# Performance work log

Measured on AMD Instinct MI355X. Metric: run time of the kernel, lower is better.

Reference implementation:

```python
import jax, jax.numpy as jnp
import numpy as np

N, E, F_IN, H, G, C = 100000, 1600000, 128, 128, 2048, 1
BN_EPS = 1e-5


def setup_inputs() -> dict:
    key = jax.random.key(0)
    ks = jax.random.split(key, 12)
    x = jax.random.normal(ks[0], (N, F_IN), dtype=jnp.float32)
    edge_index = jax.random.randint(ks[1], (2, E), 0, N, dtype=jnp.int64)
    batch = jnp.sort(jax.random.randint(ks[2], (N,), 0, G, dtype=jnp.int64))

    def xavier(k, fan_in, fan_out):
        lim = float(np.sqrt(6.0 / (fan_in + fan_out)))
        return jax.random.uniform(k, (fan_in, fan_out), jnp.float32, -lim, lim)

    return {
        "x": x, "edge_index": edge_index, "batch": batch,
        "W1": xavier(ks[3], F_IN, H), "b1": jnp.zeros((H,), jnp.float32),
        "g1": jnp.ones((H,), jnp.float32), "bt1": jnp.zeros((H,), jnp.float32),
        "W2": xavier(ks[4], H, H), "b2": jnp.zeros((H,), jnp.float32),
        "g2": jnp.ones((H,), jnp.float32), "bt2": jnp.zeros((H,), jnp.float32),
        "W3": xavier(ks[5], H, H), "b3": jnp.zeros((H,), jnp.float32),
        "g3": jnp.ones((H,), jnp.float32), "bt3": jnp.zeros((H,), jnp.float32),
        "fcw1": xavier(ks[6], H, H // 2), "fcb1": jnp.zeros((H // 2,), jnp.float32),
        "fcw2": xavier(ks[7], H // 2, C), "fcb2": jnp.zeros((C,), jnp.float32),
    }


def _gcn(x, W, b, src, dst, dis):
    # GCNConv: linear, then symmetric-normalized scatter-add with self-loops.
    xw = x @ W + b                                   # [N, H]
    norm = (dis[src] * dis[dst])[:, None]            # [E, 1]
    agg = jax.ops.segment_sum(xw[src] * norm, dst, num_segments=N)
    return agg + xw * (dis * dis)[:, None]           # self-loop term d^-1


def _bn(x, g, bt):
    mu = jnp.mean(x, axis=0)
    var = jnp.mean((x - mu) ** 2, axis=0)            # biased, training-mode BN
    return (x - mu) * jax.lax.rsqrt(var + BN_EPS) * g + bt


def reference(x, edge_index, batch, W1, b1, g1, bt1, W2, b2, g2, bt2,
              W3, b3, g3, bt3, fcw1, fcb1, fcw2, fcb2):
    src, dst = edge_index[0], edge_index[1]
    # degree with self-loops (counted on destination, as in PyG gcn_norm)
    deg = jax.ops.segment_sum(jnp.ones((E,), jnp.float32), dst, num_segments=N) + 1.0
    dis = jax.lax.rsqrt(deg)                         # deg^-1/2, deg >= 1

    h = jax.nn.relu(_bn(_gcn(x, W1, b1, src, dst, dis), g1, bt1))
    h = jax.nn.relu(_bn(_gcn(h, W2, b2, src, dst, dis), g2, bt2))
    h = jax.nn.relu(_bn(_gcn(h, W3, b3, src, dst, dis), g3, bt3))

    # global mean pool per graph
    sums = jax.ops.segment_sum(h, batch, num_segments=G)
    cnts = jax.ops.segment_sum(jnp.ones((N,), jnp.float32), batch, num_segments=G)
    pooled = sums / jnp.maximum(cnts, 1.0)[:, None]  # [G, H]

    out = jax.nn.relu(pooled @ fcw1 + fcb1)          # dropout is identity at eval
    return out @ fcw2 + fcb2                         # [G, C]
```

## Files before the change

kernel.cpp:

```cpp
#include <hip/hip_runtime.h>
#include <math.h>

#define Nn 100000
#define Ee 1600000
#define Gg 2048
#define HH 128
#define BN_EPS 1e-5f

#define NBK 196
#define NBLK_E 500
#define CHUNK4 800
#define NSTATB 256

typedef unsigned int uint32;
typedef unsigned char uchar_t;
typedef unsigned short ushort_t;
typedef __attribute__((ext_vector_type(8))) short short8_t;
typedef __attribute__((ext_vector_type(8))) unsigned short ushort8_t;
typedef __attribute__((ext_vector_type(4))) float f32x4_t;

__device__ __forceinline__ ushort_t f2bf(float f) {
    union { float f; uint32 u; } c; c.f = f;
    uint32 r = (c.u + 0x7FFFu + ((c.u >> 16) & 1u)) >> 16;
    return (ushort_t)r;
}
__device__ __forceinline__ float bflo(uint32 v) {
    union { uint32 u; float f; } c; c.u = v << 16; return c.f;
}
__device__ __forceinline__ float bfhi(uint32 v) {
    union { uint32 u; float f; } c; c.u = v & 0xFFFF0000u; return c.f;
}
__device__ __forceinline__ int q8(float f, float inv) {
    float t = f * inv;
    t = fmaxf(fminf(t, 127.f), -127.f);
    return (int)rintf(t);
}

__global__ __launch_bounds__(256) void k_count(const int* __restrict__ dst,
                                               int* __restrict__ blkhist) {
    __shared__ unsigned h[NBK];
    int tid = threadIdx.x;
    for (int i = tid; i < NBK; i += 256) h[i] = 0;
    __syncthreads();
    const int4* d4 = (const int4*)dst + blockIdx.x * CHUNK4;
    for (int i = tid; i < CHUNK4; i += 256) {
        int4 v = d4[i];
        atomicAdd(&h[v.x >> 9], 1u);
        atomicAdd(&h[v.y >> 9], 1u);
        atomicAdd(&h[v.z >> 9], 1u);
        atomicAdd(&h[v.w >> 9], 1u);
    }
    __syncthreads();
    for (int i = tid; i < NBK; i += 256)
        blkhist[blockIdx.x * NBK + i] = (int)h[i];
}

__global__ __launch_bounds__(512) void k_bscan1(const int* __restrict__ blkhist,
                                                int* __restrict__ blkoff_rel,
                                                int* __restrict__ total) {
    __shared__ int tmp[512];
    int bucket = blockIdx.x;
    int t = threadIdx.x;
    int v = (t < NBLK_E) ? blkhist[t * NBK + bucket] : 0;
    tmp[t] = v;
    __syncthreads();
    for (int off = 1; off < 512; off <<= 1) {
        int u = (t >= off) ? tmp[t - off] : 0;
        __syncthreads();
        tmp[t] += u;
        __syncthreads();
    }
    if (t < NBLK_E) blkoff_rel[t * NBK + bucket] = tmp[t] - v;
    if (t == 511) total[bucket] = tmp[t];
}

__global__ void k_bscan2(const int* __restrict__ total,
                         int* __restrict__ bucket_base) {
    __shared__ int tmp[256];
    int t = threadIdx.x;
    int v = (t < NBK) ? total[t] : 0;
    tmp[t] = v;
    __syncthreads();
    for (int off = 1; off < 256; off <<= 1) {
        int u = (t >= off) ? tmp[t - off] : 0;
        __syncthreads();
        tmp[t] += u;
        __syncthreads();
    }
    if (t < NBK) bucket_base[t] = tmp[t] - v;
}

__global__ __launch_bounds__(256) void k_fill1(const int* __restrict__ src,
                                               const int* __restrict__ dst,
                                               const int* __restrict__ bucket_base,
                                               const int* __restrict__ blkoff_rel,
                                               uint32* __restrict__ pairs) {
    __shared__ int loff[NBK];
    __shared__ unsigned lh[NBK];
    int tid = threadIdx.x;
    for (int i = tid; i < NBK; i += 256) {
        loff[i] = bucket_base[i] + blkoff_rel[blockIdx.x * NBK + i];
        lh[i] = 0;
    }
    __syncthreads();
    const int4* s4 = (const int4*)src + blockIdx.x * CHUNK4;
    const int4* d4 = (const int4*)dst + blockIdx.x * CHUNK4;
    for (int i = tid; i < CHUNK4; i += 256) {
        int4 s = s4[i];
        int4 d = d4[i];
        int b0 = d.x >> 9; int r0 = (int)atomicAdd(&lh[b0], 1u);
        pairs[loff[b0] + r0] = ((uint32)(d.x & 511) << 17) | (uint32)s.x;
        int b1 = d.y >> 9; int r1 = (int)atomicAdd(&lh[b1], 1u);
        pairs[loff[b1] + r1] = ((uint32)(d.y & 511) << 17) | (uint32)s.y;
        int b2 = d.z >> 9; int r2 = (int)atomicAdd(&lh[b2], 1u);
        pairs[loff[b2] + r2] = ((uint32)(d.z & 511) << 17) | (uint32)s.z;
        int b3 = d.w >> 9; int r3 = (int)atomicAdd(&lh[b3], 1u);
        pairs[loff[b3] + r3] = ((uint32)(d.w & 511) << 17) | (uint32)s.w;
    }
}

__global__ __launch_bounds__(1024) void k_fill2(const int* __restrict__ bucket_base,
                                                const int* __restrict__ total,
                                                const uint32* __restrict__ pairs,
                                                int* __restrict__ csr_src,
                                                int* __restrict__ rowptr,
                                                float* __restrict__ dis) {
    __shared__ unsigned lcnt[512];
    __shared__ int tmp[512];
    __shared__ int lcur[512];
    int b = blockIdx.x;
    int node0 = b * 512;
    int tid = threadIdx.x;
    for (int i = tid; i < 512; i += 1024) lcnt[i] = 0;
    __syncthreads();
    int beg = bucket_base[b];
    int endp = beg + total[b];
    for (int j = beg + tid; j < endp; j += 1024)
        atomicAdd(&lcnt[pairs[j] >> 17], 1u);
    __syncthreads();
    if (tid < 512) tmp[tid] = (int)lcnt[tid];
    __syncthreads();
    for (int off = 1; off < 512; off <<= 1) {
        int u = (tid < 512 && tid >= off) ? tmp[tid - off] : 0;
        __syncthreads();
        if (tid < 512) tmp[tid] += u;
        __syncthreads();
    }
    if (tid < 512) {
        int excl = tmp[tid] - (int)lcnt[tid];
        int n = node0 + tid;
        if (n <= Nn) rowptr[n] = beg + excl;
        if (n < Nn) dis[n] = rsqrtf((float)lcnt[tid] + 1.0f);
        lcur[tid] = beg + excl;
    }
    __syncthreads();
    for (int j = beg + tid; j < endp; j += 1024) {
        uint32 p = pairs[j];
        int dl = (int)(p >> 17);
        int s = (int)(p & 0x1FFFFu);
        int pos = atomicAdd(&lcur[dl], 1);
        csr_src[pos] = s;
    }
}

__global__ __launch_bounds__(256) void k_wprep(const float* __restrict__ W1,
                                               const float* __restrict__ W2,
                                               const float* __restrict__ W3,
                                               ushort_t* __restrict__ Wb) {
    int l = blockIdx.x >> 6, part = blockIdx.x & 63;
    const float* W = (l == 0) ? W1 : (l == 1) ? W2 : W3;
    int i = part * 256 + threadIdx.x;
    int k = i >> 7, col = i & 127;
    Wb[l * 16384 + col * 128 + k] = f2bf(W[k * 128 + col]);
}

__global__ __launch_bounds__(256) void k_gemm(const float* __restrict__ Xf,
                                              const uint32* __restrict__ Xb,
                                              const ushort_t* __restrict__ Wb,
                                              const float* __restrict__ Bv,
                                              const float* __restrict__ bnp,
                                              const float* __restrict__ dis,
                                              uchar_t* __restrict__ XW8,
                                              float* __restrict__ sc_src) {
    __shared__ ushort_t Wlds[128 * 136];
    __shared__ ushort_t Xlds[64 * 136];
    __shared__ float smax[64];
    const int tid = threadIdx.x;
    const int rowbase = blockIdx.x * 64;

#pragma unroll
    for (int it = 0; it < 8; ++it) {
        int chunk = tid + it * 256;
        int col = chunk >> 4, kg = chunk & 15;
        *(ushort8_t*)&Wlds[col * 136 + kg * 8] =
            *(const ushort8_t*)&Wb[col * 128 + kg * 8];
    }
    {
        int row = tid >> 2, q = tid & 3;
        int g = rowbase + row;
        if (bnp == nullptr) {
            const float4* Xr = (const float4*)(Xf + (size_t)g * 128);
#pragma unroll
            for (int it = 0; it < 8; ++it) {
                int c4 = q + it * 4;
                float4 v;
                if (g < Nn) v = Xr[c4];
                else { v.x = v.y = v.z = v.w = 0.f; }
                ushort4 o;
                o.x = f2bf(v.x); o.y = f2bf(v.y); o.z = f2bf(v.z); o.w = f2bf(v.w);
                *(ushort4*)&Xlds[row * 136 + c4 * 4] = o;
            }
        } else {
            const uint4* Hr = (const uint4*)(Xb + (size_t)g * 64);
#pragma unroll
            for (int it = 0; it < 4; ++it) {
                int i4 = q + it * 4;
                int c0 = i4 * 8;
                ushort8_t o;
                if (g < Nn) {
                    uint4 u = Hr[i4];
                    float4 sca = *(const float4*)&bnp[c0];
                    float4 scb = *(const float4*)&bnp[c0 + 4];
                    float4 sha = *(const float4*)&bnp[128 + c0];
                    float4 shb = *(const float4*)&bnp[128 + c0 + 4];
                    o[0] = f2bf(fmaxf(fmaf(bflo(u.x), sca.x, sha.x), 0.f));
                    o[1] = f2bf(fmaxf(fmaf(bfhi(u.x), sca.y, sha.y), 0.f));
                    o[2] = f2bf(fmaxf(fmaf(bflo(u.y), sca.z, sha.z), 0.f));
                    o[3] = f2bf(fmaxf(fmaf(bfhi(u.y), sca.w, sha.w), 0.f));
                    o[4] = f2bf(fmaxf(fmaf(bflo(u.z), scb.x, shb.x), 0.f));
                    o[5] = f2bf(fmaxf(fmaf(bfhi(u.z), scb.y, shb.y), 0.f));
                    o[6] = f2bf(fmaxf(fmaf(bflo(u.w), scb.z, shb.z), 0.f));
                    o[7] = f2bf(fmaxf(fmaf(bfhi(u.w), scb.w, shb.w), 0.f));
                } else {
                    for (int j = 0; j < 8; ++j) o[j] = 0;
                }
                *(ushort8_t*)&Xlds[row * 136 + c0] = o;
            }
        }
    }
    __syncthreads();

    const int wid = tid >> 6, lane = tid & 63;
    const int arow = wid * 16 + (lane & 15);
    const int koff = (lane >> 4) * 8;
    const int bcol = lane & 15;

    f32x4_t acc[8];
#pragma unroll
    for (int nt = 0; nt < 8; ++nt) acc[nt] = (f32x4_t){0.f, 0.f, 0.f, 0.f};

#pragma unroll
    for (int kt = 0; kt < 4; ++kt) {
        short8_t a = *(const short8_t*)&Xlds[arow * 136 + kt * 32 + koff];
#pragma unroll
        for (int nt = 0; nt < 8; ++nt) {
            short8_t b = *(const short8_t*)&Wlds[(nt * 16 + bcol) * 136 + kt * 32 + koff];
            acc[nt] = __builtin_amdgcn_mfma_f32_16x16x32_bf16(a, b, acc[nt], 0, 0, 0);
        }
    }

    int er = wid * 16 + (lane >> 4) * 4;
    int r0 = rowbase + er;
    float dv[4];
#pragma unroll
    for (int i = 0; i < 4; ++i) dv[i] = (r0 + i < Nn) ? dis[r0 + i] : 0.f;
    __syncthreads();
    float bs[8];
#pragma unroll
    for (int nt = 0; nt < 8; ++nt) bs[nt] = Bv[nt * 16 + bcol];
#pragma unroll
    for (int i = 0; i < 4; ++i) {
        float m = 0.f;
#pragma unroll
        for (int nt = 0; nt < 8; ++nt) {
            float v = (acc[nt][i] + bs[nt]) * dv[i];
            m = fmaxf(m, fabsf(v));
            Xlds[(er + i) * 136 + nt * 16 + bcol] = f2bf(v);
        }
        m = fmaxf(m, __shfl_xor(m, 1));
        m = fmaxf(m, __shfl_xor(m, 2));
        m = fmaxf(m, __shfl_xor(m, 4));
        m = fmaxf(m, __shfl_xor(m, 8));
        if (bcol == 0) smax[er + i] = m;
    }
    __syncthreads();
#pragma unroll
    for (int it = 0; it < 4; ++it) {
        int chunk = tid + it * 256;
        int row = chunk >> 4, cg = chunk & 15;
        int g = rowbase + row;
        if (g < Nn) {
            float mx = smax[row];
            float inv = (mx > 0.f) ? (127.0f / mx) : 0.f;
            uint4 u = *(const uint4*)&Xlds[row * 136 + cg * 8];
            int b0 = q8(bflo(u.x), inv), b1 = q8(bfhi(u.x), inv);
            int b2 = q8(bflo(u.y), inv), b3 = q8(bfhi(u.y), inv);
            int b4 = q8(bflo(u.z), inv), b5 = q8(bfhi(u.z), inv);
            int b6 = q8(bflo(u.w), inv), b7 = q8(bfhi(u.w), inv);
            uint2 o;
            o.x = (uint32)(b0 & 255) | ((uint32)(b1 & 255) << 8) |
                  ((uint32)(b2 & 255) << 16) | ((uint32)(b3 & 255) << 24);
            o.y = (uint32)(b4 & 255) | ((uint32)(b5 & 255) << 8) |
                  ((uint32)(b6 & 255) << 16) | ((uint32)(b7 & 255) << 24);
            *(uint2*)&XW8[(size_t)g * 128 + cg * 8] = o;
            if (cg == 0) sc_src[g] = mx * (1.0f / 127.0f);
        }
    }
}

__global__ __launch_bounds__(256) void k_agg(const uint32* __restrict__ XW32,
                                             const float* __restrict__ sc_src,
                                             const float* __restrict__ dis,
                                             const int* __restrict__ rowptr,
                                             const int* __restrict__ csr_src,
                                             uint32* __restrict__ HP32) {
    __shared__ uint2 spair[256];
    int w = threadIdx.x >> 6;
    int lane = threadIdx.x & 63;
    int half = lane >> 5, li = lane & 31;
    int node = (blockIdx.x * 4 + w) * 2 + half;
    int beg = rowptr[node], end = rowptr[node + 1];
    uint2* wpair = &spair[w * 64];
    float a0 = 0.f, a1 = 0.f, a2 = 0.f, a3 = 0.f;
    int base = beg;
    while (__any(base < end)) {
        int j = base + li;
        if (j < end) {
            int s = csr_src[j];
            float sc = sc_src[s];
            uint2 p; p.x = (uint32)s; p.y = __float_as_uint(sc);
            wpair[lane] = p;
        }
        __builtin_amdgcn_wave_barrier();
        int m = end - base; m = (m > 32) ? 32 : m;
        int k = 0;
        for (; k + 4 <= m; k += 4) {
            uint2 p0 = wpair[half * 32 + k + 0];
            uint2 p1 = wpair[half * 32 + k + 1];
            uint2 p2 = wpair[half * 32 + k + 2];
            uint2 p3 = wpair[half * 32 + k + 3];
            uint32 u0 = XW32[(size_t)p0.x * 32 + li];
            uint32 u1 = XW32[(size_t)p1.x * 32 + li];
            uint32 u2 = XW32[(size_t)p2.x * 32 + li];
            uint32 u3 = XW32[(size_t)p3.x * 32 + li];
            float c0 = __uint_as_float(p0.y);
            float c1 = __uint_as_float(p1.y);
            float c2 = __uint_as_float(p2.y);
            float c3 = __uint_as_float(p3.y);
            a0 = fmaf((float)((int)(u0 << 24) >> 24), c0, a0);
            a1 = fmaf((float)((int)(u0 << 16) >> 24), c0, a1);
            a2 = fmaf((float)((int)(u0 <<  8) >> 24), c0, a2);
            a3 = fmaf((float)((int)u0 >> 24),          c0, a3);
            a0 = fmaf((float)((int)(u1 << 24) >> 24), c1, a0);
            a1 = fmaf((float)((int)(u1 << 16) >> 24), c1, a1);
            a2 = fmaf((float)((int)(u1 <<  8) >> 24), c1, a2);
            a3 = fmaf((float)((int)u1 >> 24),          c1, a3);
            a0 = fmaf((float)((int)(u2 << 24) >> 24), c2, a0);
            a1 = fmaf((float)((int)(u2 << 16) >> 24), c2, a1);
            a2 = fmaf((float)((int)(u2 <<  8) >> 24), c2, a2);
            a3 = fmaf((float)((int)u2 >> 24),          c2, a3);
            a0 = fmaf((float)((int)(u3 << 24) >> 24), c3, a0);
            a1 = fmaf((float)((int)(u3 << 16) >> 24), c3, a1);
            a2 = fmaf((float)((int)(u3 <<  8) >> 24), c3, a2);
            a3 = fmaf((float)((int)u3 >> 24),          c3, a3);
        }
        for (; k < m; ++k) {
            uint2 p = wpair[half * 32 + k];
            uint32 u = XW32[(size_t)p.x * 32 + li];
            float sc = __uint_as_float(p.y);
            a0 = fmaf((float)((int)(u << 24) >> 24), sc, a0);
            a1 = fmaf((float)((int)(u << 16) >> 24), sc, a1);
            a2 = fmaf((float)((int)(u <<  8) >> 24), sc, a2);
            a3 = fmaf((float)((int)u >> 24),          sc, a3);
        }
        base += 32;
        __builtin_amdgcn_wave_barrier();
    }
    {
        uint32 u = XW32[(size_t)node * 32 + li];
        float sc = sc_src[node];
        a0 = fmaf((float)((int)(u << 24) >> 24), sc, a0);
        a1 = fmaf((float)((int)(u << 16) >> 24), sc, a1);
        a2 = fmaf((float)((int)(u <<  8) >> 24), sc, a2);
        a3 = fmaf((float)((int)u >> 24),          sc, a3);
    }
    float d = dis[node];
    uint2 r;
    r.x = (uint32)f2bf(a0 * d) | ((uint32)f2bf(a1 * d) << 16);
    r.y = (uint32)f2bf(a2 * d) | ((uint32)f2bf(a3 * d) << 16);
    ((uint2*)HP32)[(size_t)node * 32 + li] = r;
}

__global__ __launch_bounds__(256) void k_statsA(const uint32* __restrict__ HP32,
                                                float* __restrict__ partials) {
    const uint2* HPu2 = (const uint2*)HP32;
    int tid = threadIdx.x;
    int li = tid & 31;
    int s  = tid >> 5;
    float s0 = 0.f, s1 = 0.f, s2 = 0.f, s3 = 0.f;
    float q0 = 0.f, q1 = 0.f, q2 = 0.f, q3 = 0.f;
    for (int r = blockIdx.x * 8 + s; r < Nn; r += NSTATB * 8) {
        uint2 v = HPu2[(size_t)r * 32 + li];
        float a = bflo(v.x), b = bfhi(v.x), c = bflo(v.y), d = bfhi(v.y);
        s0 += a; s1 += b; s2 += c; s3 += d;
        q0 = fmaf(a, a, q0); q1 = fmaf(b, b, q1);
        q2 = fmaf(c, c, q2); q3 = fmaf(d, d, q3);
    }
    __shared__ float arr[8 * 256];
    float* mine = &arr[s * 256 + li * 4];
    mine[0] = s0; mine[1] = s1; mine[2] = s2; mine[3] = s3;
    mine[128] = q0; mine[129] = q1; mine[130] = q2; mine[131] = q3;
    __syncthreads();
    float tot = 0.f;
#pragma unroll
    for (int k = 0; k < 8; ++k) tot += arr[k * 256 + tid];
    partials[blockIdx.x * 256 + tid] = tot;
}

__global__ __launch_bounds__(1024) void k_statsB(const float* __restrict__ partials,
                                                 const float* __restrict__ g,
                                                 const float* __restrict__ bt,
                                                 float* __restrict__ bnp) {
    int tid = threadIdx.x;
    int sub = tid >> 8;
    int t = tid & 255;
    float acc = 0.f;
#pragma unroll 8
    for (int r = sub * 64; r < sub * 64 + 64; ++r)
        acc += partials[r * 256 + t];
    __shared__ float red[4 * 256];
    red[sub * 256 + t] = acc;
    __syncthreads();
    __shared__ float tot[256];
    if (tid < 256)
        tot[tid] = red[tid] + red[256 + tid] + red[512 + tid] + red[768 + tid];
    __syncthreads();
    if (tid < 128) {
        float mu  = tot[tid] * (1.0f / Nn);
        float var = tot[128 + tid] * (1.0f / Nn) - mu * mu;
        float sc  = g[tid] * rsqrtf(var + BN_EPS);
        bnp[tid]       = sc;
        bnp[128 + tid] = bt[tid] - mu * sc;
    }
}

__global__ __launch_bounds__(128) void k_pool_fc(const ushort_t* __restrict__ HP16,
                                                 const float* __restrict__ bnp,
                                                 const int* __restrict__ batch,
                                                 const float* __restrict__ fcw1,
                                                 const float* __restrict__ fcb1,
                                                 const float* __restrict__ fcw2,
                                                 const float* __restrict__ fcb2,
                                                 float* __restrict__ out) {
    int g = blockIdx.x;
    int t = threadIdx.x;
    int lo = 0, hi = Nn;
    while (lo < hi) { int mid = (lo + hi) >> 1; if (batch[mid] < g) lo = mid + 1; else hi = mid; }
    int start = lo;
    hi = Nn;
    while (lo < hi) { int mid = (lo + hi) >> 1; if (batch[mid] < g + 1) lo = mid + 1; else hi = mid; }
    int end = lo;

    float sc = bnp[t], sh = bnp[128 + t];
    float acc = 0.f;
    for (int i = start; i < end; ++i) {
        union { uint32 u; float f; } c;
        c.u = (uint32)HP16[(size_t)i * 128 + t] << 16;
        acc += fmaxf(fmaf(c.f, sc, sh), 0.f);
    }
    float inv = 1.0f / fmaxf((float)(end - start), 1.0f);

    __shared__ float p[128];
    __shared__ float h1[64];
    p[t] = acc * inv;
    __syncthreads();
    if (t < 64) {
        float s = fcb1[t];
        for (int k = 0; k < 128; ++k) s = fmaf(p[k], fcw1[k * 64 + t], s);
        h1[t] = fmaxf(s, 0.f);
    }
    __syncthreads();
    if (t < 64) {
        float v = h1[t] * fcw2[t];
        for (int off = 32; off > 0; off >>= 1) v += __shfl_down(v, off, 64);
        if (t == 0) out[g] = v + fcb2[0];
    }
}

extern "C" void kernel_launch(void* const* d_in, const int* in_sizes, int n_in,
                              void* d_out, int out_size, void* d_ws, size_t ws_size,
                              hipStream_t stream) {
    const float* x     = (const float*)d_in[0];
    const int*   ei    = (const int*)d_in[1];
    const int*   batch = (const int*)d_in[2];
    const float* W1  = (const float*)d_in[3];
    const float* b1  = (const float*)d_in[4];
    const float* g1  = (const float*)d_in[5];
    const float* bt1 = (const float*)d_in[6];
    const float* W2  = (const float*)d_in[7];
    const float* b2  = (const float*)d_in[8];
    const float* g2  = (const float*)d_in[9];
    const float* bt2 = (const float*)d_in[10];
    const float* W3  = (const float*)d_in[11];
    const float* b3  = (const float*)d_in[12];
    const float* g3  = (const float*)d_in[13];
    const float* bt3 = (const float*)d_in[14];
    const float* fcw1 = (const float*)d_in[15];
    const float* fcb1 = (const float*)d_in[16];
    const float* fcw2 = (const float*)d_in[17];
    const float* fcb2 = (const float*)d_in[18];
    float* out = (float*)d_out;

    uchar_t*  XW8     = (uchar_t*)d_ws;
    uint32*   HP32    = (uint32*)(XW8 + (size_t)Nn * HH);
    float*    sc_src  = (float*)(HP32 + (size_t)Nn * 64);
    float*    dis     = sc_src + Nn;
    int*      rowptr  = (int*)(dis + Nn);
    int*      blkhist = rowptr + (Nn + 1);
    int*      blkoff_rel = blkhist + NBLK_E * NBK;
    int*      total   = blkoff_rel + NBLK_E * NBK;
    int*      bucket_base = total + NBK;
    uint32*   pairs   = (uint32*)(bucket_base + NBK);
    int*      csr_src = (int*)(pairs + Ee);
    float*    partials = (float*)(csr_src + Ee);
    float*    bnp     = partials + NSTATB * 256;
    ushort_t* Wb      = (ushort_t*)(bnp + 768);

    const int* src = ei;
    const int* dst = ei + Ee;

    k_count<<<NBLK_E, 256, 0, stream>>>(dst, blkhist);
    k_wprep<<<192, 256, 0, stream>>>(W1, W2, W3, Wb);
    k_bscan1<<<NBK, 512, 0, stream>>>(blkhist, blkoff_rel, total);
    k_bscan2<<<1, 256, 0, stream>>>(total, bucket_base);
    k_fill1<<<NBLK_E, 256, 0, stream>>>(src, dst, bucket_base, blkoff_rel, pairs);
    k_fill2<<<NBK, 1024, 0, stream>>>(bucket_base, total, pairs, csr_src, rowptr, dis);

    const float* bs_[3]  = {b1, b2, b3};
    const float* gs_[3]  = {g1, g2, g3};
    const float* bts_[3] = {bt1, bt2, bt3};
    const int ngemm = (Nn + 63) / 64;
    for (int l = 0; l < 3; ++l) {
        const float* bnp_in = (l == 0) ? nullptr : (bnp + (l - 1) * 256);
        k_gemm<<<ngemm, 256, 0, stream>>>(x, HP32, Wb + l * 16384, bs_[l], bnp_in,
                                          dis, XW8, sc_src);
        k_agg<<<12500, 256, 0, stream>>>((const uint32*)XW8, sc_src, dis, rowptr,
                                         csr_src, HP32);
        k_statsA<<<NSTATB, 256, 0, stream>>>(HP32, partials);
        k_statsB<<<1, 1024, 0, stream>>>(partials, gs_[l], bts_[l], bnp + l * 256);
    }
    k_pool_fc<<<Gg, 128, 0, stream>>>((const ushort_t*)HP32, bnp + 512, batch,
                                      fcw1, fcb1, fcw2, fcb2, out);
}
```

Before: 308.9 us.

## Batch bucket scans, double rows per GEMM block, and widen stats partials

```diff
diff --git a/kernel.cpp b/kernel.cpp
--- a/kernel.cpp
+++ b/kernel.cpp
@@ -10,7 +10,7 @@
 #define NBK 196
 #define NBLK_E 500
 #define CHUNK4 800
-#define NSTATB 256
+#define NSTATB 1024
 
 typedef unsigned int uint32;
 typedef unsigned char uchar_t;
@@ -58,20 +58,36 @@
 __global__ __launch_bounds__(512) void k_bscan1(const int* __restrict__ blkhist,
                                                 int* __restrict__ blkoff_rel,
                                                 int* __restrict__ total) {
-    __shared__ int tmp[512];
-    int bucket = blockIdx.x;
+    __shared__ int tmp[512 * 9];
+    int b0 = blockIdx.x * 8;
     int t = threadIdx.x;
-    int v = (t < NBLK_E) ? blkhist[t * NBK + bucket] : 0;
-    tmp[t] = v;
+    int v[8];
+#pragma unroll
+    for (int c = 0; c < 8; ++c)
+        v[c] = (t < NBLK_E && b0 + c < NBK) ? blkhist[t * NBK + b0 + c] : 0;
+#pragma unroll
+    for (int c = 0; c < 8; ++c) tmp[t * 9 + c] = v[c];
     __syncthreads();
     for (int off = 1; off < 512; off <<= 1) {
-        int u = (t >= off) ? tmp[t - off] : 0;
-        __syncthreads();
-        tmp[t] += u;
-        __syncthreads();
-    }
-    if (t < NBLK_E) blkoff_rel[t * NBK + bucket] = tmp[t] - v;
-    if (t == 511) total[bucket] = tmp[t];
+        int u[8];
+#pragma unroll
+        for (int c = 0; c < 8; ++c)
+            u[c] = (t >= off) ? tmp[(t - off) * 9 + c] : 0;
+        __syncthreads();
+#pragma unroll
+        for (int c = 0; c < 8; ++c) tmp[t * 9 + c] += u[c];
+        __syncthreads();
+    }
+    if (t < NBLK_E) {
+#pragma unroll
+        for (int c = 0; c < 8; ++c)
+            if (b0 + c < NBK) blkoff_rel[t * NBK + b0 + c] = tmp[t * 9 + c] - v[c];
+    }
+    if (t == 511) {
+#pragma unroll
+        for (int c = 0; c < 8; ++c)
+            if (b0 + c < NBK) total[b0 + c] = tmp[511 * 9 + c];
+    }
 }
 
 __global__ void k_bscan2(const int* __restrict__ total,
@@ -186,7 +202,7 @@
     __shared__ ushort_t Xlds[64 * 136];
     __shared__ float smax[64];
     const int tid = threadIdx.x;
-    const int rowbase = blockIdx.x * 64;
+    const int rowbase0 = blockIdx.x * 128;
 
 #pragma unroll
     for (int it = 0; it < 8; ++it) {
@@ -195,115 +211,121 @@
         *(ushort8_t*)&Wlds[col * 136 + kg * 8] =
             *(const ushort8_t*)&Wb[col * 128 + kg * 8];
     }
-    {
-        int row = tid >> 2, q = tid & 3;
-        int g = rowbase + row;
-        if (bnp == nullptr) {
-            const float4* Xr = (const float4*)(Xf + (size_t)g * 128);
-#pragma unroll
-            for (int it = 0; it < 8; ++it) {
-                int c4 = q + it * 4;
-                float4 v;
-                if (g < Nn) v = Xr[c4];
-                else { v.x = v.y = v.z = v.w = 0.f; }
-                ushort4 o;
-                o.x = f2bf(v.x); o.y = f2bf(v.y); o.z = f2bf(v.z); o.w = f2bf(v.w);
-                *(ushort4*)&Xlds[row * 136 + c4 * 4] = o;
-            }
-        } else {
-            const uint4* Hr = (const uint4*)(Xb + (size_t)g * 64);
-#pragma unroll
-            for (int it = 0; it < 4; ++it) {
-                int i4 = q + it * 4;
-                int c0 = i4 * 8;
-                ushort8_t o;
-                if (g < Nn) {
-                    uint4 u = Hr[i4];
-                    float4 sca = *(const float4*)&bnp[c0];
-                    float4 scb = *(const float4*)&bnp[c0 + 4];
-                    float4 sha = *(const float4*)&bnp[128 + c0];
-                    float4 shb = *(const float4*)&bnp[128 + c0 + 4];
-                    o[0] = f2bf(fmaxf(fmaf(bflo(u.x), sca.x, sha.x), 0.f));
-                    o[1] = f2bf(fmaxf(fmaf(bfhi(u.x), sca.y, sha.y), 0.f));
-                    o[2] = f2bf(fmaxf(fmaf(bflo(u.y), sca.z, sha.z), 0.f));
-                    o[3] = f2bf(fmaxf(fmaf(bfhi(u.y), sca.w, sha.w), 0.f));
-                    o[4] = f2bf(fmaxf(fmaf(bflo(u.z), scb.x, shb.x), 0.f));
-                    o[5] = f2bf(fmaxf(fmaf(bfhi(u.z), scb.y, shb.y), 0.f));
-                    o[6] = f2bf(fmaxf(fmaf(bflo(u.w), scb.z, shb.z), 0.f));
-                    o[7] = f2bf(fmaxf(fmaf(bfhi(u.w), scb.w, shb.w), 0.f));
-                } else {
-                    for (int j = 0; j < 8; ++j) o[j] = 0;
-                }
-                *(ushort8_t*)&Xlds[row * 136 + c0] = o;
-            }
-        }
-    }
-    __syncthreads();
 
     const int wid = tid >> 6, lane = tid & 63;
     const int arow = wid * 16 + (lane & 15);
     const int koff = (lane >> 4) * 8;
     const int bcol = lane & 15;
 
-    f32x4_t acc[8];
-#pragma unroll
-    for (int nt = 0; nt < 8; ++nt) acc[nt] = (f32x4_t){0.f, 0.f, 0.f, 0.f};
-
-#pragma unroll
-    for (int kt = 0; kt < 4; ++kt) {
-        short8_t a = *(const short8_t*)&Xlds[arow * 136 + kt * 32 + koff];
-#pragma unroll
-        for (int nt = 0; nt < 8; ++nt) {
-            short8_t b = *(const short8_t*)&Wlds[(nt * 16 + bcol) * 136 + kt * 32 + koff];
-            acc[nt] = __builtin_amdgcn_mfma_f32_16x16x32_bf16(a, b, acc[nt], 0, 0, 0);
-        }
-    }
-
-    int er = wid * 16 + (lane >> 4) * 4;
-    int r0 = rowbase + er;
-    float dv[4];
-#pragma unroll
-    for (int i = 0; i < 4; ++i) dv[i] = (r0 + i < Nn) ? dis[r0 + i] : 0.f;
-    __syncthreads();
-    float bs[8];
-#pragma unroll
-    for (int nt = 0; nt < 8; ++nt) bs[nt] = Bv[nt * 16 + bcol];
-#pragma unroll
-    for (int i = 0; i < 4; ++i) {
-        float m = 0.f;
-#pragma unroll
-        for (int nt = 0; nt < 8; ++nt) {
-            float v = (acc[nt][i] + bs[nt]) * dv[i];
-            m = fmaxf(m, fabsf(v));
-            Xlds[(er + i) * 136 + nt * 16 + bcol] = f2bf(v);
-        }
-        m = fmaxf(m, __shfl_xor(m, 1));
-        m = fmaxf(m, __shfl_xor(m, 2));
-        m = fmaxf(m, __shfl_xor(m, 4));
-        m = fmaxf(m, __shfl_xor(m, 8));
-        if (bcol == 0) smax[er + i] = m;
-    }
-    __syncthreads();
-#pragma unroll
-    for (int it = 0; it < 4; ++it) {
-        int chunk = tid + it * 256;
-        int row = chunk >> 4, cg = chunk & 15;
-        int g = rowbase + row;
-        if (g < Nn) {
-            float mx = smax[row];
-            float inv = (mx > 0.f) ? (127.0f / mx) : 0.f;
-            uint4 u = *(const uint4*)&Xlds[row * 136 + cg * 8];
-            int b0 = q8(bflo(u.x), inv), b1 = q8(bfhi(u.x), inv);
-            int b2 = q8(bflo(u.y), inv), b3 = q8(bfhi(u.y), inv);
-            int b4 = q8(bflo(u.z), inv), b5 = q8(bfhi(u.z), inv);
-            int b6 = q8(bflo(u.w), inv), b7 = q8(bfhi(u.w), inv);
-            uint2 o;
-            o.x = (uint32)(b0 & 255) | ((uint32)(b1 & 255) << 8) |
-                  ((uint32)(b2 & 255) << 16) | ((uint32)(b3 & 255) << 24);
-            o.y = (uint32)(b4 & 255) | ((uint32)(b5 & 255) << 8) |
-                  ((uint32)(b6 & 255) << 16) | ((uint32)(b7 & 255) << 24);
-            *(uint2*)&XW8[(size_t)g * 128 + cg * 8] = o;
-            if (cg == 0) sc_src[g] = mx * (1.0f / 127.0f);
+    for (int sub = 0; sub < 2; ++sub) {
+        const int rowbase = rowbase0 + sub * 64;
+        if (rowbase >= Nn) break;
+        if (sub) __syncthreads();
+        {
+            int row = tid >> 2, q = tid & 3;
+            int g = rowbase + row;
+            if (bnp == nullptr) {
+                const float4* Xr = (const float4*)(Xf + (size_t)g * 128);
+#pragma unroll
+                for (int it = 0; it < 8; ++it) {
+                    int c4 = q + it * 4;
+                    float4 v;
+                    if (g < Nn) v = Xr[c4];
+                    else { v.x = v.y = v.z = v.w = 0.f; }
+                    ushort4 o;
+                    o.x = f2bf(v.x); o.y = f2bf(v.y); o.z = f2bf(v.z); o.w = f2bf(v.w);
+                    *(ushort4*)&Xlds[row * 136 + c4 * 4] = o;
+                }
+            } else {
+                const uint4* Hr = (const uint4*)(Xb + (size_t)g * 64);
+#pragma unroll
+                for (int it = 0; it < 4; ++it) {
+                    int i4 = q + it * 4;
+                    int c0 = i4 * 8;
+                    ushort8_t o;
+                    if (g < Nn) {
+                        uint4 u = Hr[i4];
+                        float4 sca = *(const float4*)&bnp[c0];
+                        float4 scb = *(const float4*)&bnp[c0 + 4];
+                        float4 sha = *(const float4*)&bnp[128 + c0];
+                        float4 shb = *(const float4*)&bnp[128 + c0 + 4];
+                        o[0] = f2bf(fmaxf(fmaf(bflo(u.x), sca.x, sha.x), 0.f));
+                        o[1] = f2bf(fmaxf(fmaf(bfhi(u.x), sca.y, sha.y), 0.f));
+                        o[2] = f2bf(fmaxf(fmaf(bflo(u.y), sca.z, sha.z), 0.f));
+                        o[3] = f2bf(fmaxf(fmaf(bfhi(u.y), sca.w, sha.w), 0.f));
+                        o[4] = f2bf(fmaxf(fmaf(bflo(u.z), scb.x, shb.x), 0.f));
+                        o[5] = f2bf(fmaxf(fmaf(bfhi(u.z), scb.y, shb.y), 0.f));
+                        o[6] = f2bf(fmaxf(fmaf(bflo(u.w), scb.z, shb.z), 0.f));
+                        o[7] = f2bf(fmaxf(fmaf(bfhi(u.w), scb.w, shb.w), 0.f));
+                    } else {
+                        for (int j = 0; j < 8; ++j) o[j] = 0;
+                    }
+                    *(ushort8_t*)&Xlds[row * 136 + c0] = o;
+                }
+            }
+        }
+        __syncthreads();
+
+        f32x4_t acc[8];
+#pragma unroll
+        for (int nt = 0; nt < 8; ++nt) acc[nt] = (f32x4_t){0.f, 0.f, 0.f, 0.f};
+
+#pragma unroll
+        for (int kt = 0; kt < 4; ++kt) {
+            short8_t a = *(const short8_t*)&Xlds[arow * 136 + kt * 32 + koff];
+#pragma unroll
+            for (int nt = 0; nt < 8; ++nt) {
+                short8_t b = *(const short8_t*)&Wlds[(nt * 16 + bcol) * 136 + kt * 32 + koff];
+                acc[nt] = __builtin_amdgcn_mfma_f32_16x16x32_bf16(a, b, acc[nt], 0, 0, 0);
+            }
+        }
+
+        int er = wid * 16 + (lane >> 4) * 4;
+        int r0 = rowbase + er;
+        float dv[4];
+#pragma unroll
+        for (int i = 0; i < 4; ++i) dv[i] = (r0 + i < Nn) ? dis[r0 + i] : 0.f;
+        __syncthreads();
+        float bs[8];
+#pragma unroll
+        for (int nt = 0; nt < 8; ++nt) bs[nt] = Bv[nt * 16 + bcol];
+#pragma unroll
+        for (int i = 0; i < 4; ++i) {
+            float m = 0.f;
+#pragma unroll
+            for (int nt = 0; nt < 8; ++nt) {
+                float v = (acc[nt][i] + bs[nt]) * dv[i];
+                m = fmaxf(m, fabsf(v));
+                Xlds[(er + i) * 136 + nt * 16 + bcol] = f2bf(v);
+            }
+            m = fmaxf(m, __shfl_xor(m, 1));
+            m = fmaxf(m, __shfl_xor(m, 2));
+            m = fmaxf(m, __shfl_xor(m, 4));
+            m = fmaxf(m, __shfl_xor(m, 8));
+            if (bcol == 0) smax[er + i] = m;
+        }
+        __syncthreads();
+#pragma unroll
+        for (int it = 0; it < 4; ++it) {
+            int chunk = tid + it * 256;
+            int row = chunk >> 4, cg = chunk & 15;
+            int g = rowbase + row;
+            if (g < Nn) {
+                float mx = smax[row];
+                float inv = (mx > 0.f) ? (127.0f / mx) : 0.f;
+                uint4 u = *(const uint4*)&Xlds[row * 136 + cg * 8];
+                int b0 = q8(bflo(u.x), inv), b1 = q8(bfhi(u.x), inv);
+                int b2 = q8(bflo(u.y), inv), b3 = q8(bfhi(u.y), inv);
+                int b4 = q8(bflo(u.z), inv), b5 = q8(bfhi(u.z), inv);
+                int b6 = q8(bflo(u.w), inv), b7 = q8(bfhi(u.w), inv);
+                uint2 o;
+                o.x = (uint32)(b0 & 255) | ((uint32)(b1 & 255) << 8) |
+                      ((uint32)(b2 & 255) << 16) | ((uint32)(b3 & 255) << 24);
+                o.y = (uint32)(b4 & 255) | ((uint32)(b5 & 255) << 8) |
+                      ((uint32)(b6 & 255) << 16) | ((uint32)(b7 & 255) << 24);
+                *(uint2*)&XW8[(size_t)g * 128 + cg * 8] = o;
+                if (cg == 0) sc_src[g] = mx * (1.0f / 127.0f);
+            }
         }
     }
 }
@@ -426,7 +448,7 @@
     int t = tid & 255;
     float acc = 0.f;
 #pragma unroll 8
-    for (int r = sub * 64; r < sub * 64 + 64; ++r)
+    for (int r = sub * 256; r < sub * 256 + 256; ++r)
         acc += partials[r * 256 + t];
     __shared__ float red[4 * 256];
     red[sub * 256 + t] = acc;
@@ -531,7 +553,7 @@
 
     k_count<<<NBLK_E, 256, 0, stream>>>(dst, blkhist);
     k_wprep<<<192, 256, 0, stream>>>(W1, W2, W3, Wb);
-    k_bscan1<<<NBK, 512, 0, stream>>>(blkhist, blkoff_rel, total);
+    k_bscan1<<<(NBK + 7) / 8, 512, 0, stream>>>(blkhist, blkoff_rel, total);
     k_bscan2<<<1, 256, 0, stream>>>(total, bucket_base);
     k_fill1<<<NBLK_E, 256, 0, stream>>>(src, dst, bucket_base, blkoff_rel, pairs);
     k_fill2<<<NBK, 1024, 0, stream>>>(bucket_base, total, pairs, csr_src, rowptr, dis);
@@ -539,7 +561,7 @@
     const float* bs_[3]  = {b1, b2, b3};
     const float* gs_[3]  = {g1, g2, g3};
     const float* bts_[3] = {bt1, bt2, bt3};
-    const int ngemm = (Nn + 63) / 64;
+    const int ngemm = (Nn + 127) / 128;
     for (int l = 0; l < 3; ++l) {
         const float* bnp_in = (l == 0) ? nullptr : (bnp + (l - 1) * 256);
         k_gemm<<<ngemm, 256, 0, stream>>>(x, HP32, Wb + l * 16384, bs_[l], bnp_in,
```

Result: slower. 323.1 us (+4.6%).
